# Optimization experiments

Measured on AMD Instinct MI355X. Metric: run time of the kernel, lower is better.

Reference implementation:

```python
import jax, jax.numpy as jnp
import numpy as np

N_ITER, N_TAPS, N_DELAY, N_SRC = 2, 4, 1, 4
EPS = 1e-3
TINY = 1e-20
BATCH, N_CHAN, N_FREQ, N_FRAMES = 2, 6, 320, 500


def mag_sq(x):
    return x.real ** 2 + x.imag ** 2


def divide(num, denom, eps):
    return num / jnp.maximum(denom, eps)


def make_xbar(X, n_taps, n_delay):
    # X: (..., c, f, n) -> X_bar: (..., c, f, t, n); tap t is X delayed by n_delay + t
    n = X.shape[-1]
    pad = [(0, 0)] * (X.ndim - 1)
    taps = [jnp.pad(X, pad + [(n_delay + t, 0)])[..., :n] for t in range(n_taps)]
    return jnp.stack(taps, axis=-2)


def background_update(W, H, C_XX, C_XbarX, eps=1e-5):
    # recompute J from W, H and input covariances (ridge-loaded solve)
    n_src = W.shape[-3]
    A1 = jnp.einsum('...sfc,...cfd->...fsd', W, C_XX)
    A2 = jnp.einsum('...sfdt,...dtfc->...fsc', H, C_XbarX)
    Am = A1 + A2
    mat = Am[..., :n_src]
    load = jnp.abs(jnp.diagonal(mat, axis1=-2, axis2=-1)).sum(axis=-1)[..., None, None]
    load = jnp.maximum(load * eps, eps) * jnp.eye(n_src, dtype=mat.dtype)
    load = jax.lax.stop_gradient(load)
    J_H = jnp.linalg.solve(mat + load, Am[..., n_src:])
    return jnp.moveaxis(J_H.conj(), -1, -3)  # (..., n_bak, f, n_src)


def iss_type1(src, Y, w, eps):
    n = Y.shape[-1]
    Ys = Y[..., src, :, :]
    vn = jnp.einsum('...cfn,...cfn,...fn->...cf', w, Y, Ys.conj()) / n
    vd = jnp.einsum('...cfn,...fn->...cf', w, mag_sq(Ys)) / n
    v = divide(vn, vd, eps)
    vs = 1.0 - 1.0 / jnp.sqrt(jnp.maximum(vd[..., src, :], eps))
    return v.at[..., src, :].set(vs.astype(v.dtype))


def iss_type2(Y, Zs, w, eps):
    vn = jnp.einsum('...cfn,...cfn,...fn->...cf', w, Y, Zs.conj())
    vd = jnp.einsum('...cfn,...fn->...cf', w, mag_sq(Zs))
    return divide(vn, vd, eps)


def iss_type3(src, tap, Y, X_bar, w, eps):
    Xst = X_bar[..., src, :, tap, :]
    vn = jnp.einsum('...cfn,...cfn,...fn->...cf', w, Y, Xst.conj())
    vd = jnp.einsum('...cfn,...fn->...cf', w, mag_sq(Xst))
    return divide(vn, vd, eps)


def mat_up1(W, H, A, v, src, eps):
    Wn = W - jnp.einsum('...cf,...fd->...cfd', v, W[..., src, :, :])
    Hn = H - jnp.einsum('...cf,...fdt->...cfdt', v, H[..., src, :, :, :])
    u = jnp.einsum('...sfc,...cf->...sf', A[..., :v.shape[-2]], v)
    u = u / (1.0 - v[..., src:src + 1, :] + eps)
    return Wn, Hn, A.at[..., src].add(u)


def mat_up2(W, J, A, v, g, eps):
    n_src = W.shape[-3]
    v2 = v[..., :n_src, :] + jnp.einsum('...sfc,...cf->...sf', W[..., n_src:], v[..., n_src:, :])
    W1 = W[..., :n_src] - jnp.einsum('...cf,...fd->...cfd', v[..., :n_src, :], g)
    Wn = jnp.concatenate([W1, W[..., n_src:]], axis=-1)
    Jn = J - jnp.einsum('...cf,...fd->...cfd', v[..., n_src:, :], g)
    Av = jnp.einsum('...sfc,...cf->...sf', A[..., :v2.shape[-2]], v2)
    gA = jnp.einsum('...fs,...sfc->...fc', g, A[..., :g.shape[-1], :, :])
    denom = 1.0 - jnp.einsum('...cf,...fc->...f', v2, gA)
    mul = denom.conj() / (mag_sq(denom) + eps)
    An = A + jnp.einsum('...sf,...fc->...sfc', Av, gA * mul[..., None])
    return Wn, Jn, An


def bak_update_vector(p, d, g, eps):
    gdg = jnp.sum(mag_sq(g) / (d + eps), axis=-2)
    gdp = jnp.sum(g.conj() * p / (d + eps), axis=-2)
    b = 1.0 - gdp
    b1 = mag_sq(b)
    a = b1 * gdg + TINY
    beta = (-b1 + jnp.sqrt(b1 ** 2 + 4.0 * a)) / (2.0 * a)
    ell1 = beta * b
    ell2 = (1.0 / jnp.sqrt(eps + gdg)).astype(ell1.dtype)
    ell = jnp.where(b1 > eps ** 2, ell1, ell2)
    return (p - ell[..., None, :] * g) / (d + eps)


def bak_update(bak, Y, Z, X, W, J, A, w, eps):
    n_src, n_freq, n_frames = Y.shape[-3:]
    n_chan = X.shape[-3]
    Zs = Z[..., bak, :, :] + X[..., n_src + bak, :, :]
    norm = 1.0 / n_frames
    ones = jnp.ones(w.shape[:-3] + (n_chan - n_src, n_freq, n_frames), w.dtype)
    wz = jnp.concatenate([w, ones], axis=-3)
    YZ = jnp.concatenate([Y, Z], axis=-3)
    p = jnp.einsum('...cfn,...cfn,...fn->...cf', YZ, wz, Zs.conj()) * norm
    d = jnp.einsum('...cfn,...fn->...cf', wz, mag_sq(Zs)) * norm
    A2 = jnp.concatenate([A, jnp.einsum('...sfc,...cfd->...sfd', A, W[..., n_src:])], axis=-1)
    g = jnp.einsum('...fs,...sfc->...cf', J[..., bak, :, :], A2).conj()
    v = bak_update_vector(p, d, g, eps)
    YZ = YZ - jnp.einsum('...cf,...fn->...cfn', v, Zs)
    return v, YZ[..., :n_src, :, :], YZ[..., n_src:, :, :]


def iss_updates(Y, X, X_bar, W, H, A, w, J, Z, eps):
    n_src = Y.shape[-3]
    n_chan = X.shape[-3]
    n_taps = X_bar.shape[-2]
    n_bak = n_chan - n_src
    # 1) background rows (structured type-2 updates)
    for bak in range(n_bak):
        v, Y, Z = bak_update(bak, Y, Z, X, W, J, A, w, eps)
        g = J[..., bak, :, :]
        W, J, A = mat_up2(W, J, A, v, g, eps)
    # 2) source directions (type 1)
    for src in range(n_src):
        v = iss_type1(src, Y, w, eps)
        Y = Y - jnp.einsum('...cf,...fn->...cfn', v, Y[..., src, :, :])
        W, H, A = mat_up1(W, H, A, v, src, eps)
    # 3) background directions (type 2)
    for bak in range(n_bak):
        v = iss_type2(Y, Z[..., bak, :, :], w, eps)
        Y = Y - jnp.einsum('...cf,...fn->...cfn', v, Z[..., bak, :, :])
        W = W.at[..., :n_src].add(-jnp.einsum('...cf,...fd->...cfd', v, J[..., bak, :, :]))
        W = W.at[..., n_src + bak].add(v)
    if n_bak > 0:
        # keep A consistent: A = inv(W1 + W2 J) per frequency
        Binv = W[..., :n_src] + jnp.einsum('...sfc,...cfd->...sfd', W[..., n_src:], J)
        A = jnp.moveaxis(jnp.linalg.inv(jnp.moveaxis(Binv, -2, -3)), -3, -2)
    # 4) dereverberation taps (type 3)
    for src in range(n_chan):
        for tap in range(n_taps):
            v = iss_type3(src, tap, Y, X_bar, w, eps)
            Y = Y - jnp.einsum('...cf,...fn->...cfn', v, X_bar[..., src, :, tap, :])
            H = H.at[..., src, tap].add(v)
    return Y, Z, W, H, J, A


def _forward(X):
    batch = X.shape[:-3]
    n_chan, n_freq, n_frames = X.shape[-3:]
    n_src = N_SRC
    X_bar = make_xbar(X, N_TAPS, N_DELAY)
    W = jnp.broadcast_to(jnp.eye(n_src, n_chan, dtype=X.dtype)[:, None, :], batch + (n_src, n_freq, n_chan))
    H = jnp.zeros(batch + (n_src, n_freq, n_chan, N_TAPS), X.dtype)
    A = jnp.broadcast_to(jnp.eye(n_src, dtype=X.dtype)[:, None, :], batch + (n_src, n_freq, n_src))
    # initialize background demixing J from input second-order statistics
    C_XX = jnp.einsum('...cfn,...dfn->...cfd', X, X.conj()) / n_frames
    C_XbarX = jnp.einsum('...dftn,...cfn->...dtfc', X_bar, X.conj()) / n_frames
    J = background_update(W, H, C_XX, C_XbarX)
    Y = X[..., :n_src, :, :]
    Z = jnp.einsum('...cfd,...dfn->...cfn', J, X[..., :n_src, :, :]) - X[..., n_src:, :, :]
    for _ in range(N_ITER):
        # Gauss (time-varying) source-model weights, shared across frequencies
        w = 1.0 / jnp.maximum(jnp.mean(mag_sq(Y), axis=-2, keepdims=True), EPS)
        w = jnp.broadcast_to(w, Y.shape)
        Y, Z, W, H, J, A = iss_updates(Y, X, X_bar, W, H, A, w, J, Z, EPS)
    return Y


def setup_inputs():
    key = jax.random.key(0)
    k1, k2 = jax.random.split(key)
    shape = (BATCH, N_CHAN, N_FREQ, N_FRAMES)
    return {"X_real": jax.random.normal(k1, shape, jnp.float32),
            "X_imag": jax.random.normal(k2, shape, jnp.float32)}


def reference(X_real, X_imag):
    X = jax.lax.complex(X_real, X_imag)
    return _forward(X)
```

## Files before the change

kernel.cpp:

```cpp
#include <hip/hip_runtime.h>

#define NFR 500
#define NFQ 320
#define NB  2
#define NC  6
#define NS  4
#define NBK 2
#define NT  4
#define NDLY 1
#define EPSF 1e-3f
#define TINYF 1e-20f

#define NP   512
#define XPAD 8
#define XLEN (XPAD + NP)
#define NCH  8
#define FPC  (NFQ / NCH)

typedef float f2 __attribute__((ext_vector_type(2)));

__device__ __forceinline__ f2 mk2(float r, float i){ f2 t; t.x = r; t.y = i; return t; }
__device__ __forceinline__ f2 cmul(f2 a, f2 b){ return a.xx*b + a.yy*mk2(-b.y, b.x); }
__device__ __forceinline__ f2 cmulc(f2 a, f2 b){ return b.xx*a + b.yy*mk2(a.y, -a.x); }
__device__ __forceinline__ f2 conjc(f2 a){ return mk2(a.x, -a.y); }
__device__ __forceinline__ float cmag2(f2 a){ return a.x*a.x + a.y*a.y; }
__device__ __forceinline__ f2 cinv(f2 a){ float m = a.x*a.x + a.y*a.y; return mk2(a.x/m, -a.y/m); }

#define DPPF(x, ctrl) __int_as_float(__builtin_amdgcn_mov_dpp(__float_as_int(x), (ctrl), 0xF, 0xF, true))
__device__ __forceinline__ float wred64(float x){
  x += DPPF(x, 0x111);
  x += DPPF(x, 0x112);
  x += DPPF(x, 0x114);
  x += DPPF(x, 0x118);
  x += DPPF(x, 0x142);
  x += DPPF(x, 0x143);
  return __int_as_float(__builtin_amdgcn_readlane(__float_as_int(x), 63));
}

__global__ __launch_bounds__(512) void k_wpartX(const float* __restrict__ Xr,
                                                const float* __restrict__ Xi,
                                                float* __restrict__ wacc)
{
  const int bs = blockIdx.x / NCH;
  const int ch = blockIdx.x % NCH;
  const int n  = threadIdx.x;
  if (n >= NFR) return;
  const int b = bs / NS, s = bs % NS;
  const size_t rowb = ((size_t)(b*NC + s)*NFQ)*NFR + n;
  float acc = 0.f;
  for (int ff = 0; ff < FPC; ++ff) {
    size_t idx = rowb + (size_t)(ch*FPC + ff)*NFR;
    float xr = Xr[idx], xi = Xi[idx];
    acc += xr*xr + xi*xi;
  }
  wacc[((size_t)(ch*NB*NS + bs))*NFR + n] = acc;
}

__global__ __launch_bounds__(512) void k_wpartY(const f2* __restrict__ Yg,
                                                float* __restrict__ wacc)
{
  const int bs = blockIdx.x / NCH;
  const int ch = blockIdx.x % NCH;
  const int n  = threadIdx.x;
  if (n >= NFR) return;
  const f2* row = Yg + (size_t)bs*NFQ*NFR + n;
  f2 acc2 = mk2(0.f,0.f);
  for (int ff = 0; ff < FPC; ++ff)
    { f2 y = row[(size_t)(ch*FPC + ff)*NFR]; acc2 += y*y; }
  wacc[((size_t)(ch*NB*NS + bs))*NFR + n] = acc2.x + acc2.y;
}

__global__ __launch_bounds__(512) void k_wfin(const float* __restrict__ wacc,
                                              float* __restrict__ wg)
{
  const int bs = blockIdx.x;
  const int n  = threadIdx.x;
  if (n >= NFR) return;
  float a = 0.f;
#pragma unroll
  for (int ch = 0; ch < NCH; ++ch) a += wacc[((size_t)(ch*NB*NS + bs))*NFR + n];
  wg[bs*NFR + n] = 1.0f / fmaxf(a * (1.0f/(float)NFQ), EPSF);
}

__global__ __launch_bounds__(256, 3) void k_iter(
  const float* __restrict__ Xr, const float* __restrict__ Xi,
  f2* __restrict__ Yg, f2* __restrict__ Zg,
  f2* __restrict__ Wg, f2* __restrict__ Jg, f2* __restrict__ Ag,
  const float* __restrict__ wg, float* __restrict__ outR,
  const int first, const int last)
{
  __shared__ f2 sXp[NC][XLEN];
  __shared__ f2 sZ[NBK][NP];
  __shared__ f2 sS[NP];
  __shared__ f2 sW[NS][NC];
  __shared__ f2 sJ[NBK][NS];
  __shared__ f2 sA[NS][NS];
  __shared__ f2 sB[NS][2*NS];
  __shared__ f2 sv[NC], sg[NC], sgo[NS];
  __shared__ float sd[NC];
  __shared__ f2 sp[NC];
  __shared__ f2 sAv[NS], sgA[NS], sWsrc[NC];

  const int bf = blockIdx.x;
  const int b = bf / NFQ, f = bf % NFQ;
  const int tid = threadIdx.x, wv = tid >> 6, lane = tid & 63;

  f2 yreg[8];
  float wreg[8];

  for (int c = 0; c < NC; ++c) {
    const size_t base = ((size_t)(b*NC + c)*NFQ + f)*NFR;
    for (int j = tid; j < XLEN; j += 256) {
      int n = j - XPAD;
      sXp[c][j] = (n >= 0 && n < NFR) ? mk2(Xr[base+n], Xi[base+n]) : mk2(0.f,0.f);
    }
  }

  if (first) {
    __syncthreads();
    for (int p = wv; p < NS*NC; p += 4) {
      int s = p / NC, d = p % NC;
      f2 ar2 = mk2(0.f,0.f), ai2 = mk2(0.f,0.f);
#pragma unroll
      for (int i = 0; i < 8; ++i) {
        int n = lane + 64*i;
        f2 xs = sXp[s][XPAD+n], xd = sXp[d][XPAD+n];
        ar2 += xs * xd;
        ai2 += xs.yx * mk2(xd.x, -xd.y);
      }
      float ar = wred64(ar2.x + ar2.y), ai = wred64(ai2.x + ai2.y);
      if (lane == 0) sB[s][d] = mk2(ar*(1.f/NFR), ai*(1.f/NFR));
    }
    if (tid >= 192 && tid < 192 + NS*NC) {
      int t = tid - 192; sW[t/NC][t%NC] = (t/NC == t%NC) ? mk2(1.f,0.f) : mk2(0.f,0.f);
    } else if (tid >= 224 && tid < 224 + NS*NS) {
      int t = tid - 224; sA[t/NS][t%NS] = (t/NS == t%NS) ? mk2(1.f,0.f) : mk2(0.f,0.f);
    }
    __syncthreads();
    if (tid == 0) {
      float dsum = 0.f;
      for (int s = 0; s < NS; ++s) dsum += sqrtf(cmag2(sB[s][s]));
      float load = fmaxf(dsum*1e-5f, 1e-5f);
      for (int s = 0; s < NS; ++s) sB[s][s].x += load;
      for (int col = 0; col < NS; ++col) {
        int piv = col; float best = cmag2(sB[col][col]);
        for (int r = col+1; r < NS; ++r) { float m = cmag2(sB[r][col]); if (m > best){best=m; piv=r;} }
        if (piv != col) for (int k = col; k < NC; ++k) { f2 t=sB[col][k]; sB[col][k]=sB[piv][k]; sB[piv][k]=t; }
        f2 ip = cinv(sB[col][col]);
        for (int k = col; k < NC; ++k) sB[col][k] = cmul(sB[col][k], ip);
        for (int r = 0; r < NS; ++r) if (r != col) {
          f2 fac = sB[r][col];
          for (int k = col; k < NC; ++k) sB[r][k] -= cmul(fac, sB[col][k]);
        }
      }
      for (int k = 0; k < NBK; ++k)
        for (int s = 0; s < NS; ++s) sJ[k][s] = conjc(sB[s][NS+k]);
    }
    __syncthreads();
    for (int n = tid; n < NP; n += 256) {
      f2 x0 = sXp[0][XPAD+n], x1 = sXp[1][XPAD+n], x2 = sXp[2][XPAD+n], x3 = sXp[3][XPAD+n];
      f2 a0 = -sXp[NS+0][XPAD+n];
      a0 += cmul(sJ[0][0], x0); a0 += cmul(sJ[0][1], x1);
      a0 += cmul(sJ[0][2], x2); a0 += cmul(sJ[0][3], x3);
      f2 a1 = -sXp[NS+1][XPAD+n];
      a1 += cmul(sJ[1][0], x0); a1 += cmul(sJ[1][1], x1);
      a1 += cmul(sJ[1][2], x2); a1 += cmul(sJ[1][3], x3);
      sZ[0][n] = a0; sZ[1][n] = a1;
    }
    {
      const int bs = b*NS + wv;
#pragma unroll
      for (int i = 0; i < 8; ++i) {
        int n = lane + 64*i;
        yreg[i] = sXp[wv][XPAD+n];
        wreg[i] = (n < NFR) ? wg[bs*NFR + n] : 0.f;
      }
    }
    __syncthreads();
  } else {
    for (int k = 0; k < NBK; ++k) {
      const size_t zb = ((size_t)(b*NBK + k)*NFQ + f)*NFR;
      for (int n = tid; n < NP; n += 256) sZ[k][n] = (n < NFR) ? Zg[zb+n] : mk2(0.f,0.f);
    }
    {
      const size_t yb = ((size_t)(b*NS + wv)*NFQ + f)*NFR;
      const int bs = b*NS + wv;
#pragma unroll
      for (int i = 0; i < 8; ++i) {
        int n = lane + 64*i;
        if (n < NFR) { yreg[i] = Yg[yb+n]; wreg[i] = wg[bs*NFR + n]; }
        else         { yreg[i] = mk2(0.f,0.f); wreg[i] = 0.f; }
      }
    }
    if (tid < NS*NC) sW[tid/NC][tid%NC] = Wg[((size_t)(b*NS + tid/NC)*NFQ + f)*NC + tid%NC];
    else if (tid < NS*NC + NBK*NS) { int t=tid-NS*NC; sJ[t/NS][t%NS] = Jg[((size_t)(b*NBK+t/NS)*NFQ+f)*NS + t%NS]; }
    else if (tid < NS*NC + NBK*NS + NS*NS) { int t=tid-NS*NC-NBK*NS; sA[t/NS][t%NS] = Ag[((size_t)(b*NS+t/NS)*NFQ+f)*NS + t%NS]; }
    __syncthreads();
  }

  f2 vl0 = mk2(0.f,0.f), vl1 = mk2(0.f,0.f), vl2 = mk2(0.f,0.f);
  f2 vl3 = mk2(0.f,0.f), vl4 = mk2(0.f,0.f), vl5 = mk2(0.f,0.f);
#define V2T(t) (vl##t + cmul(sW[t][NS+0], vl4) + cmul(sW[t][NS+1], vl5))

  for (int bak = 0; bak < NBK; ++bak) {
    if (bak > 0 && tid < 16) {
      int s = tid >> 2, c = tid & 3;
      f2 v20 = V2T(0), v21 = V2T(1), v22 = V2T(2), v23 = V2T(3);
      f2 den = mk2(1.f,0.f);
      den -= cmul(v20, sgA[0]); den -= cmul(v21, sgA[1]);
      den -= cmul(v22, sgA[2]); den -= cmul(v23, sgA[3]);
      float m2 = cmag2(den) + EPSF;
      f2 mul = mk2(den.x/m2, -den.y/m2);
      sA[s][c] += cmul(sAv[s], cmul(sgA[c], mul));
    }
    __syncthreads();

    f2 zs[8];
    {
      f2 pr2 = mk2(0.f,0.f), pi2 = mk2(0.f,0.f), dd2 = mk2(0.f,0.f);
#pragma unroll
      for (int i = 0; i < 8; ++i) {
        int n = lane+64*i;
        zs[i] = sZ[bak][n] + sXp[NS+bak][XPAD+n];
        f2 wy = wreg[i]*yreg[i];
        pr2 += wy * zs[i];
        pi2 += wy.yx * mk2(zs[i].x, -zs[i].y);
        dd2 += (wreg[i]*zs[i]) * zs[i];
      }
      float pr = wred64(pr2.x+pr2.y), pi = wred64(pi2.x+pi2.y), dd = wred64(dd2.x+dd2.y);
      if (lane == 0) { sp[wv] = mk2(pr*(1.f/NFR), pi*(1.f/NFR)); sd[wv] = dd*(1.f/NFR); }
      if (wv < NBK) {
        f2 qr2 = mk2(0.f,0.f), qi2 = mk2(0.f,0.f), qd2 = mk2(0.f,0.f);
#pragma unroll
        for (int i = 0; i < 8; ++i) {
          f2 y = sZ[wv][lane+64*i];
          qr2 += y * zs[i];
          qi2 += y.yx * mk2(zs[i].x, -zs[i].y);
          qd2 += zs[i]*zs[i];
        }
        float qr = wred64(qr2.x+qr2.y), qi = wred64(qi2.x+qi2.y), qd = wred64(qd2.x+qd2.y);
        if (lane == 0) { sp[NS+wv] = mk2(qr*(1.f/NFR), qi*(1.f/NFR)); sd[NS+wv] = qd*(1.f/NFR); }
      }
    }
    if (tid < NC) {
      int c = tid; f2 acc = mk2(0.f,0.f);
      for (int s = 0; s < NS; ++s) {
        f2 a2;
        if (c < NS) a2 = sA[s][c];
        else {
          a2 = mk2(0.f,0.f);
          for (int k = 0; k < NS; ++k) a2 += cmul(sA[s][k], sW[k][c]);
        }
        acc += cmul(sJ[bak][s], a2);
      }
      sg[c] = conjc(acc);
    } else if (tid >= 8 && tid < 8+NS) {
      sgo[tid-8] = sJ[bak][tid-8];
    }
    __syncthreads();

    {
      float gdg = 0.f; f2 gdp = mk2(0.f,0.f);
#pragma unroll
      for (int c = 0; c < NC; ++c) {
        f2 gc = sg[c]; float id = 1.0f/(sd[c] + EPSF);
        gdg += cmag2(gc) * id;
        gdp += id * cmulc(sp[c], gc);
      }
      f2 bb = mk2(1.0f - gdp.x, -gdp.y);
      float b1 = cmag2(bb);
      float a = b1*gdg + TINYF;
      float beta = (-b1 + sqrtf(b1*b1 + 4.0f*a)) / (2.0f*a);
      f2 ell = (b1 > EPSF*EPSF) ? (beta*bb) : mk2(1.0f/sqrtf(EPSF + gdg), 0.f);
#define CALCV(c) ((1.0f/(sd[c] + EPSF)) * (sp[c] - cmul(ell, sg[c])))
      vl0 = CALCV(0); vl1 = CALCV(1); vl2 = CALCV(2);
      vl3 = CALCV(3); vl4 = CALCV(4); vl5 = CALCV(5);
#undef CALCV
    }
    {
      f2 vc  = (wv == 0) ? vl0 : (wv == 1) ? vl1 : (wv == 2) ? vl2 : vl3;
#pragma unroll
      for (int i = 0; i < 8; ++i) yreg[i] -= cmul(vc, zs[i]);
      if (wv < NBK) {
        f2 v2c = (wv == 0) ? vl4 : vl5;
#pragma unroll
        for (int i = 0; i < 8; ++i) sZ[wv][lane+64*i] -= cmul(v2c, zs[i]);
      }
    }
    __syncthreads();

    if (tid < NS) {
      f2 v20 = V2T(0), v21 = V2T(1), v22 = V2T(2), v23 = V2T(3);
      f2 acc = cmul(sA[tid][0], v20);
      acc += cmul(sA[tid][1], v21);
      acc += cmul(sA[tid][2], v22);
      acc += cmul(sA[tid][3], v23);
      sAv[tid] = acc;
    } else if (tid < 2*NS) {
      int c = tid - NS; f2 acc = mk2(0.f,0.f);
#pragma unroll
      for (int s = 0; s < NS; ++s) acc += cmul(sgo[s], sA[s][c]);
      sgA[c] = acc;
    } else if (tid < 2*NS + 16) {
      int idx = tid - 2*NS; int cc = idx >> 2, d = idx & 3;
      f2 vcc = (cc == 0) ? vl0 : (cc == 1) ? vl1 : (cc == 2) ? vl2 : vl3;
      sW[cc][d] -= cmul(vcc, sgo[d]);
    } else if (tid < 2*NS + 16 + 8) {
      int idx = tid - 2*NS - 16; int k = idx >> 2, d = idx & 3;
      f2 vk = (k == 0) ? vl4 : vl5;
      sJ[k][d] -= cmul(vk, sgo[d]);
    }
    __syncthreads();
  }

  for (int src = 0; src < NS; ++src) {
    if (wv == src) {
#pragma unroll
      for (int i = 0; i < 8; ++i) sS[lane+64*i] = yreg[i];
    }
    if (tid < NC) sWsrc[tid] = sW[src][tid];
    if (src == 0) {
      if (tid < 16) {
        int s = tid >> 2, c = tid & 3;
        f2 v20 = V2T(0), v21 = V2T(1), v22 = V2T(2), v23 = V2T(3);
        f2 den = mk2(1.f,0.f);
        den -= cmul(v20, sgA[0]); den -= cmul(v21, sgA[1]);
        den -= cmul(v22, sgA[2]); den -= cmul(v23, sgA[3]);
        float m2 = cmag2(den) + EPSF;
        f2 mul = mk2(den.x/m2, -den.y/m2);
        sA[s][c] += cmul(sAv[s], cmul(sgA[c], mul));
      }
    } else if (tid >= 8 && tid < 8+NS) {
      int r = tid - 8, prev = src - 1;
      f2 acc = mk2(0.f,0.f);
#pragma unroll
      for (int c = 0; c < NS; ++c) acc += cmul(sA[r][c], sv[c]);
      float den = 1.0f - sv[prev].x + EPSF;
      sA[r][prev] += (1.0f/den) * acc;
    }
    __syncthreads();

    {
      f2 ys[8];
      f2 nr2 = mk2(0.f,0.f), ni2 = mk2(0.f,0.f), dd2 = mk2(0.f,0.f);
#pragma unroll
      for (int i = 0; i < 8; ++i) {
        ys[i] = sS[lane+64*i];
        f2 wy = wreg[i]*yreg[i];
        nr2 += wy * ys[i];
        ni2 += wy.yx * mk2(ys[i].x, -ys[i].y);
        dd2 += (wreg[i]*ys[i]) * ys[i];
      }
      float nr = wred64(nr2.x+nr2.y)*(1.f/NFR);
      float ni = wred64(ni2.x+ni2.y)*(1.f/NFR);
      float dd = wred64(dd2.x+dd2.y)*(1.f/NFR);
      f2 vc;
      if (wv == src) vc = mk2(1.0f - 1.0f/sqrtf(fmaxf(dd, EPSF)), 0.f);
      else           vc = (1.0f/fmaxf(dd, EPSF)) * mk2(nr, ni);
      if (lane == 0) sv[wv] = vc;
#pragma unroll
      for (int i = 0; i < 8; ++i) yreg[i] -= cmul(vc, ys[i]);
      if (lane < NC) sW[wv][lane] -= cmul(vc, sWsrc[lane]);
    }
    __syncthreads();
  }

  {
    f2 pr0=mk2(0,0), pi0=mk2(0,0), dd0=mk2(0,0);
    f2 pr1=mk2(0,0), pi1=mk2(0,0), dd1=mk2(0,0);
    f2 crr=mk2(0,0), cri=mk2(0,0);
    f2 z0c[8], z1c[8];
#pragma unroll
    for (int i = 0; i < 8; ++i) {
      f2 z0 = sZ[0][lane+64*i], z1 = sZ[1][lane+64*i];
      z0c[i] = z0; z1c[i] = z1;
      f2 wy = wreg[i]*yreg[i];
      f2 wz0 = wreg[i]*z0;
      pr0 += wy * z0;  pi0 += wy.yx * mk2(z0.x, -z0.y);  dd0 += wz0 * z0;
      pr1 += wy * z1;  pi1 += wy.yx * mk2(z1.x, -z1.y);  dd1 += (wreg[i]*z1) * z1;
      crr += wz0 * z1; cri += wz0.yx * mk2(z1.x, -z1.y);
    }
    float P0r = wred64(pr0.x+pr0.y), P0i = wred64(pi0.x+pi0.y), D0 = wred64(dd0.x+dd0.y);
    float P1r = wred64(pr1.x+pr1.y), P1i = wred64(pi1.x+pi1.y), D1 = wred64(dd1.x+dd1.y);
    float Rr  = wred64(crr.x+crr.y), Ri  = wred64(cri.x+cri.y);
    f2 v0 = (1.0f/fmaxf(D0, EPSF)) * mk2(P0r, P0i);
    f2 P1c = mk2(P1r, P1i) - cmul(v0, mk2(Rr, Ri));
    f2 v1 = (1.0f/fmaxf(D1, EPSF)) * P1c;
#pragma unroll
    for (int i = 0; i < 8; ++i) yreg[i] -= cmul(v0, z0c[i]) + cmul(v1, z1c[i]);
    if (lane < NS) sW[wv][lane] -= cmul(v0, sJ[0][lane]) + cmul(v1, sJ[1][lane]);
    else if (lane == NS)   sW[wv][NS+0] += v0;
    else if (lane == NS+1) sW[wv][NS+1] += v1;
  }
  __syncthreads();

  if (!last) {
    if (tid < 16) {
      int s = tid >> 2, d = tid & 3;
      f2 acc = sW[s][d];
      acc += cmul(sW[s][NS+0], sJ[0][d]);
      acc += cmul(sW[s][NS+1], sJ[1][d]);
      sB[s][d] = acc;
      sB[s][NS+d] = (s==d) ? mk2(1.f,0.f) : mk2(0.f,0.f);
    }
    __syncthreads();
    if (tid == 0) {
      for (int col = 0; col < NS; ++col) {
        int piv = col; float best = cmag2(sB[col][col]);
        for (int r = col+1; r < NS; ++r) { float m = cmag2(sB[r][col]); if (m > best) { best = m; piv = r; } }
        if (piv != col) for (int k = 0; k < 2*NS; ++k) { f2 t = sB[col][k]; sB[col][k] = sB[piv][k]; sB[piv][k] = t; }
        f2 ip = cinv(sB[col][col]);
        for (int k = 0; k < 2*NS; ++k) sB[col][k] = cmul(sB[col][k], ip);
        for (int r = 0; r < NS; ++r) if (r != col) {
          f2 fac = sB[r][col];
          for (int k = 0; k < 2*NS; ++k) sB[r][k] -= cmul(fac, sB[col][k]);
        }
      }
    }
  }

  {
#pragma unroll 1
    for (int src = 0; src < NC; ++src) {
      const f2* __restrict__ xrow = &sXp[src][0];
#pragma unroll
      for (int tap = 0; tap < NT; ++tap) {
        const int xoff = XPAD - (NDLY + tap) + lane;
        f2 xs[8];
        f2 nr2 = mk2(0.f,0.f), ni2 = mk2(0.f,0.f), dd2 = mk2(0.f,0.f);
#pragma unroll
        for (int i = 0; i < 8; ++i) {
          xs[i] = xrow[xoff + 64*i];
          f2 wy = wreg[i]*yreg[i];
          nr2 += wy * xs[i];
          ni2 += wy.yx * mk2(xs[i].x, -xs[i].y);
          dd2 += (wreg[i]*xs[i]) * xs[i];
        }
        float nr = wred64(nr2.x+nr2.y), ni = wred64(ni2.x+ni2.y), dd = wred64(dd2.x+dd2.y);
        f2 vc = (1.0f/fmaxf(dd, EPSF)) * mk2(nr, ni);
#pragma unroll
        for (int i = 0; i < 8; ++i) yreg[i] -= cmul(vc, xs[i]);
      }
    }
  }

  {
    const size_t yb = ((size_t)(b*NS + wv)*NFQ + f)*NFR;
    if (last) {
#pragma unroll
      for (int i = 0; i < 8; ++i) { int n = lane+64*i; if (n < NFR) outR[yb+n] = yreg[i].x; }
    } else {
#pragma unroll
      for (int i = 0; i < 8; ++i) { int n = lane+64*i; if (n < NFR) Yg[yb+n] = yreg[i]; }
    }
  }
  if (!last) {
    __syncthreads();
    for (int k = 0; k < NBK; ++k) {
      const size_t zb = ((size_t)(b*NBK+k)*NFQ + f)*NFR;
      for (int n = tid; n < NFR; n += 256) Zg[zb+n] = sZ[k][n];
    }
    if (tid < NS*NC) Wg[((size_t)(b*NS + tid/NC)*NFQ + f)*NC + tid%NC] = sW[tid/NC][tid%NC];
    else if (tid < NS*NC + NBK*NS) { int t = tid - NS*NC; Jg[((size_t)(b*NBK + t/NS)*NFQ + f)*NS + t%NS] = sJ[t/NS][t%NS]; }
    else if (tid < NS*NC + NBK*NS + NS*NS) { int t = tid - NS*NC - NBK*NS; Ag[((size_t)(b*NS + t/NS)*NFQ + f)*NS + t%NS] = sB[t/NS][NS + t%NS]; }
  }
#undef V2T
}

extern "C" void kernel_launch(void* const* d_in, const int* in_sizes, int n_in,
                              void* d_out, int out_size, void* d_ws, size_t ws_size,
                              hipStream_t stream)
{
  (void)in_sizes; (void)n_in; (void)out_size; (void)ws_size;
  const float* Xr = (const float*)d_in[0];
  const float* Xi = (const float*)d_in[1];
  float* outR = (float*)d_out;

  char* ws = (char*)d_ws;
  size_t off = 0;
  f2* Yg = (f2*)(ws + off); off += (size_t)NB*NS*NFQ*NFR*sizeof(f2);
  f2* Zg = (f2*)(ws + off); off += (size_t)NB*NBK*NFQ*NFR*sizeof(f2);
  f2* Wg = (f2*)(ws + off); off += (size_t)NB*NS*NFQ*NC*sizeof(f2);
  f2* Jg = (f2*)(ws + off); off += (size_t)NB*NBK*NFQ*NS*sizeof(f2);
  f2* Ag = (f2*)(ws + off); off += (size_t)NB*NS*NFQ*NS*sizeof(f2);
  float* wacc = (float*)(ws + off); off += (size_t)NCH*NB*NS*NFR*sizeof(float);
  float* wg   = (float*)(ws + off); off += (size_t)NB*NS*NFR*sizeof(float);

  k_wpartX<<<NB*NS*NCH, 512, 0, stream>>>(Xr, Xi, wacc);
  k_wfin<<<NB*NS, 512, 0, stream>>>(wacc, wg);
  k_iter<<<NB*NFQ, 256, 0, stream>>>(Xr, Xi, Yg, Zg, Wg, Jg, Ag, wg, outR, 1, 0);
  k_wpartY<<<NB*NS*NCH, 512, 0, stream>>>(Yg, wacc);
  k_wfin<<<NB*NS, 512, 0, stream>>>(wacc, wg);
  k_iter<<<NB*NFQ, 256, 0, stream>>>(Xr, Xi, Yg, Zg, Wg, Jg, Ag, wg, outR, 0, 1);
}
```

Before: 113.6 us.

## Double-buffer ISS source updates and pair tap updates to cut barriers

Double-buffers the source row and W-source row across the type-1 ISS loop so that each source step needs one barrier instead of two. The next source's row is staged by the owning wavefront inside the loop. One barrier in the background loop is also dropped. The type-3 tap loop now processes two taps per pass, computing the cross-correlation between adjacent taps so the second tap's coefficient can be corrected algebraically instead of doing a separate reduction pass. This saves shared-memory passes and sequential reductions, at the cost of more registers and more wave reductions per pass.

```diff
diff --git a/kernel.cpp b/kernel.cpp
--- a/kernel.cpp
+++ b/kernel.cpp
@@ -91,15 +91,18 @@
 {
   __shared__ f2 sXp[NC][XLEN];
   __shared__ f2 sZ[NBK][NP];
-  __shared__ f2 sS[NP];
+  __shared__ f2 sS[2][NP];
   __shared__ f2 sW[NS][NC];
   __shared__ f2 sJ[NBK][NS];
   __shared__ f2 sA[NS][NS];
   __shared__ f2 sB[NS][2*NS];
-  __shared__ f2 sv[NC], sg[NC], sgo[NS];
+  __shared__ f2 svb[2][NS];
+  __shared__ f2 sg[NC], sgo[NS];
   __shared__ float sd[NC];
   __shared__ f2 sp[NC];
-  __shared__ f2 sAv[NS], sgA[NS], sWsrc[NC];
+  __shared__ f2 sAv[NS], sgA[NS];
+  __shared__ f2 sWsrc[2][NC];
+  __shared__ f2 sW45[NS][2];
 
   const int bf = blockIdx.x;
   const int b = bf / NFQ, f = bf % NFQ;
@@ -203,17 +206,19 @@
 #define V2T(t) (vl##t + cmul(sW[t][NS+0], vl4) + cmul(sW[t][NS+1], vl5))
 
   for (int bak = 0; bak < NBK; ++bak) {
-    if (bak > 0 && tid < 16) {
-      int s = tid >> 2, c = tid & 3;
-      f2 v20 = V2T(0), v21 = V2T(1), v22 = V2T(2), v23 = V2T(3);
-      f2 den = mk2(1.f,0.f);
-      den -= cmul(v20, sgA[0]); den -= cmul(v21, sgA[1]);
-      den -= cmul(v22, sgA[2]); den -= cmul(v23, sgA[3]);
-      float m2 = cmag2(den) + EPSF;
-      f2 mul = mk2(den.x/m2, -den.y/m2);
-      sA[s][c] += cmul(sAv[s], cmul(sgA[c], mul));
-    }
-    __syncthreads();
+    if (bak > 0) {
+      if (tid < 16) {
+        int s = tid >> 2, c = tid & 3;
+        f2 v20 = V2T(0), v21 = V2T(1), v22 = V2T(2), v23 = V2T(3);
+        f2 den = mk2(1.f,0.f);
+        den -= cmul(v20, sgA[0]); den -= cmul(v21, sgA[1]);
+        den -= cmul(v22, sgA[2]); den -= cmul(v23, sgA[3]);
+        float m2 = cmag2(den) + EPSF;
+        f2 mul = mk2(den.x/m2, -den.y/m2);
+        sA[s][c] += cmul(sAv[s], cmul(sgA[c], mul));
+      }
+      __syncthreads();
+    }
 
     f2 zs[8];
     {
@@ -287,8 +292,6 @@
         for (int i = 0; i < 8; ++i) sZ[wv][lane+64*i] -= cmul(v2c, zs[i]);
       }
     }
-    __syncthreads();
-
     if (tid < NS) {
       f2 v20 = V2T(0), v21 = V2T(1), v22 = V2T(2), v23 = V2T(3);
       f2 acc = cmul(sA[tid][0], v20);
@@ -304,25 +307,66 @@
     } else if (tid < 2*NS + 16) {
       int idx = tid - 2*NS; int cc = idx >> 2, d = idx & 3;
       f2 vcc = (cc == 0) ? vl0 : (cc == 1) ? vl1 : (cc == 2) ? vl2 : vl3;
-      sW[cc][d] -= cmul(vcc, sgo[d]);
-    } else if (tid < 2*NS + 16 + 8) {
+      f2 nv = sW[cc][d] - cmul(vcc, sgo[d]);
+      sW[cc][d] = nv;
+      if (bak == NBK-1 && cc == 0) sWsrc[0][d] = nv;
+    } else if (tid < 2*NS + 24) {
       int idx = tid - 2*NS - 16; int k = idx >> 2, d = idx & 3;
       f2 vk = (k == 0) ? vl4 : vl5;
       sJ[k][d] -= cmul(vk, sgo[d]);
+    } else if (bak == NBK-1) {
+      if (tid == 40)      sWsrc[0][4] = sW[0][4];
+      else if (tid == 41) sWsrc[0][5] = sW[0][5];
+      else if (tid >= 48 && tid < 56) {
+        int t = (tid-48) >> 1, j = (tid-48) & 1;
+        sW45[t][j] = sW[t][NS+j];
+      }
+    }
+    if (bak == NBK-1 && wv == 0) {
+#pragma unroll
+      for (int i = 0; i < 8; ++i) sS[0][lane+64*i] = yreg[i];
     }
     __syncthreads();
   }
 
   for (int src = 0; src < NS; ++src) {
-    if (wv == src) {
-#pragma unroll
-      for (int i = 0; i < 8; ++i) sS[lane+64*i] = yreg[i];
-    }
-    if (tid < NC) sWsrc[tid] = sW[src][tid];
+    const int par = src & 1;
+    {
+      f2 ys[8];
+      f2 nr2 = mk2(0.f,0.f), ni2 = mk2(0.f,0.f), dd2 = mk2(0.f,0.f);
+#pragma unroll
+      for (int i = 0; i < 8; ++i) {
+        ys[i] = sS[par][lane+64*i];
+        f2 wy = wreg[i]*yreg[i];
+        nr2 += wy * ys[i];
+        ni2 += wy.yx * mk2(ys[i].x, -ys[i].y);
+        dd2 += (wreg[i]*ys[i]) * ys[i];
+      }
+      float nr = wred64(nr2.x+nr2.y)*(1.f/NFR);
+      float ni = wred64(ni2.x+ni2.y)*(1.f/NFR);
+      float dd = wred64(dd2.x+dd2.y)*(1.f/NFR);
+      f2 vc;
+      if (wv == src) vc = mk2(1.0f - 1.0f/sqrtf(fmaxf(dd, EPSF)), 0.f);
+      else           vc = (1.0f/fmaxf(dd, EPSF)) * mk2(nr, ni);
+      if (lane == 0) svb[par][wv] = vc;
+#pragma unroll
+      for (int i = 0; i < 8; ++i) yreg[i] -= cmul(vc, ys[i]);
+      if (lane < NC) {
+        f2 nw = sW[wv][lane] - cmul(vc, sWsrc[par][lane]);
+        sW[wv][lane] = nw;
+        if (wv == src+1) sWsrc[par^1][lane] = nw;
+      }
+      if (wv == src+1) {
+#pragma unroll
+        for (int i = 0; i < 8; ++i) sS[par^1][lane+64*i] = yreg[i];
+      }
+    }
     if (src == 0) {
       if (tid < 16) {
         int s = tid >> 2, c = tid & 3;
-        f2 v20 = V2T(0), v21 = V2T(1), v22 = V2T(2), v23 = V2T(3);
+#define V2S(t) (vl##t + cmul(sW45[t][0], vl4) + cmul(sW45[t][1], vl5))
+        f2 v20 = V2S(0), v21 = V2S(1), v22 = V2S(2), v23 = V2S(3);
+#undef V2S
         f2 den = mk2(1.f,0.f);
         den -= cmul(v20, sgA[0]); den -= cmul(v21, sgA[1]);
         den -= cmul(v22, sgA[2]); den -= cmul(v23, sgA[3]);
@@ -334,33 +378,9 @@
       int r = tid - 8, prev = src - 1;
       f2 acc = mk2(0.f,0.f);
 #pragma unroll
-      for (int c = 0; c < NS; ++c) acc += cmul(sA[r][c], sv[c]);
-      float den = 1.0f - sv[prev].x + EPSF;
+      for (int c = 0; c < NS; ++c) acc += cmul(sA[r][c], svb[par^1][c]);
+      float den = 1.0f - svb[par^1][prev].x + EPSF;
       sA[r][prev] += (1.0f/den) * acc;
-    }
-    __syncthreads();
-
-    {
-      f2 ys[8];
-      f2 nr2 = mk2(0.f,0.f), ni2 = mk2(0.f,0.f), dd2 = mk2(0.f,0.f);
-#pragma unroll
-      for (int i = 0; i < 8; ++i) {
-        ys[i] = sS[lane+64*i];
-        f2 wy = wreg[i]*yreg[i];
-        nr2 += wy * ys[i];
-        ni2 += wy.yx * mk2(ys[i].x, -ys[i].y);
-        dd2 += (wreg[i]*ys[i]) * ys[i];
-      }
-      float nr = wred64(nr2.x+nr2.y)*(1.f/NFR);
-      float ni = wred64(ni2.x+ni2.y)*(1.f/NFR);
-      float dd = wred64(dd2.x+dd2.y)*(1.f/NFR);
-      f2 vc;
-      if (wv == src) vc = mk2(1.0f - 1.0f/sqrtf(fmaxf(dd, EPSF)), 0.f);
-      else           vc = (1.0f/fmaxf(dd, EPSF)) * mk2(nr, ni);
-      if (lane == 0) sv[wv] = vc;
-#pragma unroll
-      for (int i = 0; i < 8; ++i) yreg[i] -= cmul(vc, ys[i]);
-      if (lane < NC) sW[wv][lane] -= cmul(vc, sWsrc[lane]);
     }
     __syncthreads();
   }
@@ -424,22 +444,36 @@
     for (int src = 0; src < NC; ++src) {
       const f2* __restrict__ xrow = &sXp[src][0];
 #pragma unroll
-      for (int tap = 0; tap < NT; ++tap) {
-        const int xoff = XPAD - (NDLY + tap) + lane;
-        f2 xs[8];
-        f2 nr2 = mk2(0.f,0.f), ni2 = mk2(0.f,0.f), dd2 = mk2(0.f,0.f);
+      for (int tp = 0; tp < 2; ++tp) {
+        const int t0 = 2*tp;
+        const int xoff = XPAD - (NDLY + t0) + lane;
+        f2 xa[8], xb[8];
+        f2 pa_r=mk2(0,0), pa_i=mk2(0,0), da=mk2(0,0);
+        f2 pb_r=mk2(0,0), pb_i=mk2(0,0), db=mk2(0,0);
+        f2 rr=mk2(0,0), ri=mk2(0,0);
 #pragma unroll
         for (int i = 0; i < 8; ++i) {
-          xs[i] = xrow[xoff + 64*i];
+          xa[i] = xrow[xoff + 64*i];
+          xb[i] = xrow[xoff - 1 + 64*i];
           f2 wy = wreg[i]*yreg[i];
-          nr2 += wy * xs[i];
-          ni2 += wy.yx * mk2(xs[i].x, -xs[i].y);
-          dd2 += (wreg[i]*xs[i]) * xs[i];
+          f2 wxa = wreg[i]*xa[i];
+          pa_r += wy * xa[i];
+          pa_i += wy.yx * mk2(xa[i].x, -xa[i].y);
+          da   += wxa * xa[i];
+          pb_r += wy * xb[i];
+          pb_i += wy.yx * mk2(xb[i].x, -xb[i].y);
+          db   += (wreg[i]*xb[i]) * xb[i];
+          rr   += wxa * xb[i];
+          ri   += wxa.yx * mk2(xb[i].x, -xb[i].y);
         }
-        float nr = wred64(nr2.x+nr2.y), ni = wred64(ni2.x+ni2.y), dd = wred64(dd2.x+dd2.y);
-        f2 vc = (1.0f/fmaxf(dd, EPSF)) * mk2(nr, ni);
-#pragma unroll
-        for (int i = 0; i < 8; ++i) yreg[i] -= cmul(vc, xs[i]);
+        float Par = wred64(pa_r.x+pa_r.y), Pai = wred64(pa_i.x+pa_i.y), Da = wred64(da.x+da.y);
+        float Pbr = wred64(pb_r.x+pb_r.y), Pbi = wred64(pb_i.x+pb_i.y), Db = wred64(db.x+db.y);
+        float Rr  = wred64(rr.x+rr.y),     Ri  = wred64(ri.x+ri.y);
+        f2 v0 = (1.0f/fmaxf(Da, EPSF)) * mk2(Par, Pai);
+        f2 Pb = mk2(Pbr, Pbi) - cmul(v0, mk2(Rr, Ri));
+        f2 v1 = (1.0f/fmaxf(Db, EPSF)) * Pb;
+#pragma unroll
+        for (int i = 0; i < 8; ++i) yreg[i] -= cmul(v0, xa[i]) + cmul(v1, xb[i]);
       }
     }
   }
```

After: 115.5 us. About the same (+1.6%).
